# Performance work log

Measured on AMD Instinct MI355X. Metric: run time of the kernel, lower is better.

## Reference

```python
import jax, jax.numpy as jnp
import numpy as np

N_NODES = 50000


def gcn_conv(x, W, b, src, dst, n_nodes):
    # Linear transform first (PyG GCNConv): [N, out]
    h = x @ W
    # Add self-loops
    loop = jnp.arange(n_nodes, dtype=src.dtype)
    s = jnp.concatenate([src, loop])
    d = jnp.concatenate([dst, loop])
    # Symmetric normalization: deg counted at destination with unit weights
    deg = jax.ops.segment_sum(jnp.ones_like(d, dtype=h.dtype), d, num_segments=n_nodes)
    dinv = jnp.where(deg > 0, jax.lax.rsqrt(deg), 0.0)
    norm = dinv[s] * dinv[d]  # [E+N]
    # Gather source features, scale, scatter-add to destinations
    msgs = h[s] * norm[:, None]
    out = jax.ops.segment_sum(msgs, d, num_segments=n_nodes)
    return out + b


def setup_inputs() -> dict:
    key = jax.random.key(0)
    k1, k2, k3, k4, k5 = jax.random.split(key, 5)
    in_c, out_c = 512, 128
    x = jax.random.normal(k1, (N_NODES, in_c), dtype=jnp.float32)
    edge_index = jax.random.randint(k2, (2, 800000), 0, N_NODES, dtype=jnp.int64)
    glorot = 1.0 / np.sqrt(in_c)
    W_mu = jax.random.uniform(k3, (in_c, out_c), jnp.float32, -glorot, glorot)
    W_logstd = jax.random.uniform(k4, (in_c, out_c), jnp.float32, -glorot, glorot)
    b_mu = jnp.zeros((out_c,), jnp.float32)
    b_logstd = jnp.zeros((out_c,), jnp.float32)
    return {"x": x, "edge_index": edge_index, "W_mu": W_mu, "b_mu": b_mu,
            "W_logstd": W_logstd, "b_logstd": b_logstd}


def reference(x, edge_index, W_mu, b_mu, W_logstd, b_logstd):
    src, dst = edge_index[0], edge_index[1]
    mu = gcn_conv(x, W_mu, b_mu, src, dst, N_NODES)
    logstd = gcn_conv(x, W_logstd, b_logstd, src, dst, N_NODES)
    return mu, logstd
```

## Files before the change

### kernel.cpp

```cpp
#include <hip/hip_runtime.h>

#define NN 50000
#define NE 800000
#define KC 512
#define OC 256
#define NB_SCAN 196

typedef float f32x4 __attribute__((ext_vector_type(4)));
typedef short bf16x8 __attribute__((ext_vector_type(8)));

__device__ __forceinline__ unsigned f2bf(float f) {
    union { float f; unsigned u; } v; v.f = f;
    return (v.u + 0x7FFFu + ((v.u >> 16) & 1u)) >> 16;
}
__device__ __forceinline__ float bf2f(unsigned short b) {
    union { unsigned u; float f; } v; v.u = ((unsigned)b) << 16;
    return v.f;
}

__global__ __launch_bounds__(256) void count_deg_kernel(const int* __restrict__ ei,
                                                        int* __restrict__ deg) {
    int e = blockIdx.x * 256 + threadIdx.x;
    if (e < NE) atomicAdd(&deg[ei[NE + e]], 1);
}

__global__ __launch_bounds__(256) void scan_part_kernel(const int* __restrict__ deg,
                                                        int* __restrict__ partial) {
    int tid = threadIdx.x;
    int i = blockIdx.x * 256 + tid;
    int v = (i < NN) ? deg[i] : 0;
#pragma unroll
    for (int off = 32; off > 0; off >>= 1) v += __shfl_down(v, off, 64);
    __shared__ int wsum[4];
    if ((tid & 63) == 0) wsum[tid >> 6] = v;
    __syncthreads();
    if (tid == 0) partial[blockIdx.x] = wsum[0] + wsum[1] + wsum[2] + wsum[3];
}

__global__ __launch_bounds__(256) void scan_block_kernel(const int* __restrict__ partial,
                                                         int* __restrict__ blockoff) {
    __shared__ int lds[256];
    int tid = threadIdx.x;
    int v = (tid < NB_SCAN) ? partial[tid] : 0;
    lds[tid] = v;
    __syncthreads();
    for (int off = 1; off < 256; off <<= 1) {
        int t = (tid >= off) ? lds[tid - off] : 0;
        __syncthreads();
        lds[tid] += t;
        __syncthreads();
    }
    if (tid < NB_SCAN) blockoff[tid] = lds[tid] - v;
}

__global__ __launch_bounds__(256) void scan_apply_kernel(const int* __restrict__ deg,
                                                         const int* __restrict__ blockoff,
                                                         int* __restrict__ row_start,
                                                         int* __restrict__ cursor,
                                                         float* __restrict__ dinv) {
    int tid = threadIdx.x;
    int lane = tid & 63;
    int w = tid >> 6;
    int i = blockIdx.x * 256 + tid;
    int d = (i < NN) ? deg[i] : 0;
    int v = d;
#pragma unroll
    for (int off = 1; off < 64; off <<= 1) {
        int t = __shfl_up(v, off, 64);
        if (lane >= off) v += t;
    }
    __shared__ int wsum[4];
    if (lane == 63) wsum[w] = v;
    __syncthreads();
    int wof = 0;
    for (int k = 0; k < w; ++k) wof += wsum[k];
    int excl = blockoff[blockIdx.x] + wof + v - d;
    if (i < NN) {
        row_start[i] = excl;
        cursor[i] = excl;
        dinv[i] = rsqrtf((float)(d + 1));
    }
    if (i == NN - 1) row_start[NN] = excl + d;
}

__global__ __launch_bounds__(256) void scatter_kernel(const int* __restrict__ ei,
                                                      int* __restrict__ cursor,
                                                      int* __restrict__ csr_src) {
    int e = blockIdx.x * 256 + threadIdx.x;
    if (e < NE) {
        int d = ei[NE + e];
        int pos = atomicAdd(&cursor[d], 1);
        csr_src[pos] = ei[e];
    }
}

__global__ __launch_bounds__(256) void convw_kernel(const float* __restrict__ Wmu,
                                                    const float* __restrict__ Wls,
                                                    uint4* __restrict__ Wc) {
    int idx = blockIdx.x * 256 + threadIdx.x;
    int kb = idx >> 10;
    int rem = idx & 1023;
    int wf = rem >> 6;
    int lane = rem & 63;
    int g4 = lane >> 4;
    int i16 = lane & 15;
    int col = (wf >> 2) * 64 + (wf & 3) * 16 + i16;
    int k0 = kb * 32 + g4 * 8;
    const float* Wsrc = (col < 128) ? (Wmu + col) : (Wls + (col - 128));
    unsigned o[4];
#pragma unroll
    for (int p = 0; p < 4; ++p) {
        float lo = Wsrc[(size_t)(k0 + 2 * p) * 128];
        float hi = Wsrc[(size_t)(k0 + 2 * p + 1) * 128];
        o[p] = f2bf(lo) | (f2bf(hi) << 16);
    }
    uint4 v;
    v.x = o[0]; v.y = o[1]; v.z = o[2]; v.w = o[3];
    Wc[idx] = v;
}

__global__ __launch_bounds__(256, 8) void gemm_kernel(const float* __restrict__ x,
                                                      const uint4* __restrict__ Wc,
                                                      const float* __restrict__ dinv,
                                                      unsigned short* __restrict__ hs) {
    __shared__ __align__(16) float Af[2][32 * 64];

    int tid = threadIdx.x;
    int lane = tid & 63;
    int w = tid >> 6;
    int r0 = blockIdx.x * 32;
    int i16 = lane & 15;
    int g4 = lane >> 4;

    const float* srcp[2];
#pragma unroll
    for (int j = 0; j < 2; ++j) {
        int r = (w * 2 + j) * 4 + (lane >> 4);
        int gr = r0 + r;
        if (gr > NN - 1) gr = NN - 1;
        int cp = (lane & 15) >> 1;
        int mp = (lane & 1) * 4;
        int c = cp ^ (r & 7);
        int m = mp ^ (((r >> 3) & 1) * 4);
        srcp[j] = x + (size_t)gr * KC + c * 8 + m;
    }
    auto dmaA = [&](int buf, int S) {
#pragma unroll
        for (int j = 0; j < 2; ++j) {
            __builtin_amdgcn_global_load_lds(
                (const __attribute__((address_space(1))) void*)(srcp[j] + S * 64),
                (__attribute__((address_space(3))) void*)&Af[buf][(w * 2 + j) * 256], 16, 0, 0);
        }
    };

    auto readA = [&](int buf, int ks, int fr) -> bf16x8 {
        int r = fr * 16 + i16;
        int c = ks * 4 + g4;
        int cc = c ^ (r & 7);
        int mo = ((r >> 3) & 1) * 4;
        const float* p = &Af[buf][r * 64 + cc * 8];
        f32x4 lo = *(const f32x4*)(p + mo);
        f32x4 hi = *(const f32x4*)(p + (mo ^ 4));
        unsigned o0, o1, o2, o3;
        asm("v_cvt_pk_bf16_f32 %0, %1, %2" : "=v"(o0) : "v"(lo.x), "v"(lo.y));
        asm("v_cvt_pk_bf16_f32 %0, %1, %2" : "=v"(o1) : "v"(lo.z), "v"(lo.w));
        asm("v_cvt_pk_bf16_f32 %0, %1, %2" : "=v"(o2) : "v"(hi.x), "v"(hi.y));
        asm("v_cvt_pk_bf16_f32 %0, %1, %2" : "=v"(o3) : "v"(hi.z), "v"(hi.w));
        union { unsigned u[4]; bf16x8 v; } res;
        res.u[0] = o0; res.u[1] = o1; res.u[2] = o2; res.u[3] = o3;
        return res.v;
    };

    const uint4* wbase = Wc + (size_t)(w * 4) * 64 + lane;
    uint4 bb[2][4];
    auto loadB = [&](int dbuf, int kb) {
#pragma unroll
        for (int fc = 0; fc < 4; ++fc) bb[dbuf][fc] = wbase[kb * 1024 + fc * 64];
    };

    f32x4 acc[2][4];
    f32x4 zz = {0.f, 0.f, 0.f, 0.f};
#pragma unroll
    for (int a = 0; a < 2; ++a)
#pragma unroll
        for (int b = 0; b < 4; ++b) acc[a][b] = zz;

    dmaA(0, 0);
    loadB(0, 0);
    __syncthreads();

#pragma unroll
    for (int S = 0; S < 8; ++S) {
        if (S < 7) dmaA((S + 1) & 1, S + 1);
#pragma unroll
        for (int ks = 0; ks < 2; ++ks) {
            const int kb = S * 2 + ks;
            const int cur = kb & 1;
            if (kb < 15) loadB(cur ^ 1, kb + 1);
            bf16x8 af0 = readA(S & 1, ks, 0);
            bf16x8 af1 = readA(S & 1, ks, 1);
#pragma unroll
            for (int fc = 0; fc < 4; ++fc) {
                bf16x8 bfrag = *(const bf16x8*)&bb[cur][fc];
                acc[0][fc] = __builtin_amdgcn_mfma_f32_16x16x32_bf16(af0, bfrag, acc[0][fc], 0, 0, 0);
                acc[1][fc] = __builtin_amdgcn_mfma_f32_16x16x32_bf16(af1, bfrag, acc[1][fc], 0, 0, 0);
            }
        }
        if (S < 7) __syncthreads();
    }

#pragma unroll
    for (int fr = 0; fr < 2; ++fr) {
#pragma unroll
        for (int r = 0; r < 4; ++r) {
            int gr = r0 + fr * 16 + g4 * 4 + r;
            if (gr < NN) {
                float dv = dinv[gr];
#pragma unroll
                for (int fc = 0; fc < 4; ++fc) {
                    int col = w * 64 + fc * 16 + i16;
                    hs[(size_t)gr * OC + col] = (unsigned short)f2bf(acc[fr][fc][r] * dv);
                }
            }
        }
    }
}

__global__ __launch_bounds__(256) void aggregate_kernel(const unsigned short* __restrict__ hs,
                                                        const int* __restrict__ row_start,
                                                        const int* __restrict__ csr_src,
                                                        const float* __restrict__ dinv,
                                                        const float* __restrict__ bmu,
                                                        const float* __restrict__ bls,
                                                        float* __restrict__ out) {
    int tid = threadIdx.x;
    int lane = tid & 63;
    int node = blockIdx.x * 4 + (tid >> 6);

    const unsigned short* hrow = hs + lane * 4;
    float acc0, acc1, acc2, acc3;
    {
        ushort4 v = *(const ushort4*)&hrow[(size_t)node * OC];
        acc0 = bf2f(v.x);
        acc1 = bf2f(v.y);
        acc2 = bf2f(v.z);
        acc3 = bf2f(v.w);
    }
    int rs = row_start[node], re = row_start[node + 1];
    int e = rs;
    for (; e + 8 <= re; e += 8) {
        int s[8];
#pragma unroll
        for (int q = 0; q < 8; ++q) s[q] = csr_src[e + q];
        ushort4 v[8];
#pragma unroll
        for (int q = 0; q < 8; ++q) v[q] = *(const ushort4*)&hrow[(size_t)s[q] * OC];
#pragma unroll
        for (int q = 0; q < 8; ++q) {
            acc0 += bf2f(v[q].x);
            acc1 += bf2f(v[q].y);
            acc2 += bf2f(v[q].z);
            acc3 += bf2f(v[q].w);
        }
    }
    if (e + 4 <= re) {
        int s[4];
#pragma unroll
        for (int q = 0; q < 4; ++q) s[q] = csr_src[e + q];
        ushort4 v[4];
#pragma unroll
        for (int q = 0; q < 4; ++q) v[q] = *(const ushort4*)&hrow[(size_t)s[q] * OC];
#pragma unroll
        for (int q = 0; q < 4; ++q) {
            acc0 += bf2f(v[q].x);
            acc1 += bf2f(v[q].y);
            acc2 += bf2f(v[q].z);
            acc3 += bf2f(v[q].w);
        }
        e += 4;
    }
    for (; e < re; ++e) {
        int s0 = csr_src[e];
        ushort4 v0 = *(const ushort4*)&hrow[(size_t)s0 * OC];
        acc0 += bf2f(v0.x);
        acc1 += bf2f(v0.y);
        acc2 += bf2f(v0.z);
        acc3 += bf2f(v0.w);
    }
    float dn = dinv[node];
    if (lane < 32) {
        f32x4 b = *(const f32x4*)&bmu[lane * 4];
        f32x4 r;
        r.x = acc0 * dn + b.x;
        r.y = acc1 * dn + b.y;
        r.z = acc2 * dn + b.z;
        r.w = acc3 * dn + b.w;
        __builtin_nontemporal_store(r, (f32x4*)(out + (size_t)node * 128 + lane * 4));
    } else {
        f32x4 b = *(const f32x4*)&bls[(lane - 32) * 4];
        f32x4 r;
        r.x = acc0 * dn + b.x;
        r.y = acc1 * dn + b.y;
        r.z = acc2 * dn + b.z;
        r.w = acc3 * dn + b.w;
        __builtin_nontemporal_store(
            r, (f32x4*)(out + (size_t)NN * 128 + (size_t)node * 128 + (lane - 32) * 4));
    }
}

extern "C" void kernel_launch(void* const* d_in, const int* in_sizes, int n_in,
                              void* d_out, int out_size, void* d_ws, size_t ws_size,
                              hipStream_t stream) {
    const float* x = (const float*)d_in[0];
    const int* ei = (const int*)d_in[1];
    const float* Wmu = (const float*)d_in[2];
    const float* bmu = (const float*)d_in[3];
    const float* Wls = (const float*)d_in[4];
    const float* bls = (const float*)d_in[5];
    float* out = (float*)d_out;

    char* ws = (char*)d_ws;
    size_t off = 0;
    auto alloc = [&](size_t bytes) {
        void* p = ws + off;
        off += (bytes + 255) & ~(size_t)255;
        return p;
    };
    unsigned short* hs = (unsigned short*)alloc((size_t)NN * OC * sizeof(unsigned short));
    uint4* Wc = (uint4*)alloc((size_t)16384 * 16);
    int* deg = (int*)alloc((size_t)NN * sizeof(int));
    int* row_start = (int*)alloc((size_t)(NN + 1) * sizeof(int));
    int* cursor = (int*)alloc((size_t)NN * sizeof(int));
    int* csr_src = (int*)alloc((size_t)NE * sizeof(int));
    float* dinv = (float*)alloc((size_t)NN * sizeof(float));
    int* partial = (int*)alloc((size_t)NB_SCAN * sizeof(int));
    int* blockoff = (int*)alloc((size_t)NB_SCAN * sizeof(int));

    hipMemsetAsync(deg, 0, (size_t)NN * sizeof(int), stream);

    count_deg_kernel<<<(NE + 255) / 256, 256, 0, stream>>>(ei, deg);
    scan_part_kernel<<<NB_SCAN, 256, 0, stream>>>(deg, partial);
    scan_block_kernel<<<1, 256, 0, stream>>>(partial, blockoff);
    scan_apply_kernel<<<NB_SCAN, 256, 0, stream>>>(deg, blockoff, row_start, cursor, dinv);
    scatter_kernel<<<(NE + 255) / 256, 256, 0, stream>>>(ei, cursor, csr_src);
    convw_kernel<<<64, 256, 0, stream>>>(Wmu, Wls, Wc);
    gemm_kernel<<<(NN + 31) / 32, 256, 0, stream>>>(x, Wc, dinv, hs);
    aggregate_kernel<<<NN / 4, 256, 0, stream>>>(hs, row_start, csr_src, dinv, bmu, bls, out);
}
```

Baseline: 204.0 us.

## Load GEMM A fragments directly from global into registers, dropping LDS staging

The GEMM kernel no longer stages x tiles through shared memory with global_load_lds and barriers. Each wave now loads its own A fragments straight from global memory into registers, double-buffered across k-steps alongside the B fragments, and converts them to bf16 before the MFMA. This removes the LDS traffic and the block-wide syncs, but all four waves now load the same A rows redundantly, so more global/L2 traffic. Register pressure also rises, and launch bounds are relaxed from 8 to 4 waves-per-EU to accommodate it.

```diff
diff --git a/kernel.cpp b/kernel.cpp
--- a/kernel.cpp
+++ b/kernel.cpp
@@ -119,12 +119,10 @@
     Wc[idx] = v;
 }
 
-__global__ __launch_bounds__(256, 8) void gemm_kernel(const float* __restrict__ x,
+__global__ __launch_bounds__(256, 4) void gemm_kernel(const float* __restrict__ x,
                                                       const uint4* __restrict__ Wc,
                                                       const float* __restrict__ dinv,
                                                       unsigned short* __restrict__ hs) {
-    __shared__ __align__(16) float Af[2][32 * 64];
-
     int tid = threadIdx.x;
     int lane = tid & 63;
     int w = tid >> 6;
@@ -132,35 +130,28 @@
     int i16 = lane & 15;
     int g4 = lane >> 4;
 
-    const float* srcp[2];
-#pragma unroll
-    for (int j = 0; j < 2; ++j) {
-        int r = (w * 2 + j) * 4 + (lane >> 4);
-        int gr = r0 + r;
-        if (gr > NN - 1) gr = NN - 1;
-        int cp = (lane & 15) >> 1;
-        int mp = (lane & 1) * 4;
-        int c = cp ^ (r & 7);
-        int m = mp ^ (((r >> 3) & 1) * 4);
-        srcp[j] = x + (size_t)gr * KC + c * 8 + m;
-    }
-    auto dmaA = [&](int buf, int S) {
-#pragma unroll
-        for (int j = 0; j < 2; ++j) {
-            __builtin_amdgcn_global_load_lds(
-                (const __attribute__((address_space(1))) void*)(srcp[j] + S * 64),
-                (__attribute__((address_space(3))) void*)&Af[buf][(w * 2 + j) * 256], 16, 0, 0);
-        }
+    int gr0 = r0 + i16;
+    if (gr0 > NN - 1) gr0 = NN - 1;
+    int gr1 = r0 + 16 + i16;
+    if (gr1 > NN - 1) gr1 = NN - 1;
+    const float* xg0 = x + (size_t)gr0 * KC + g4 * 8;
+    const float* xg1 = x + (size_t)gr1 * KC + g4 * 8;
+    const uint4* wbase = Wc + (size_t)(w * 4) * 64 + lane;
+
+    f32x4 a0l[2], a0h[2], a1l[2], a1h[2];
+    uint4 bb[2][4];
+
+    auto loadA = [&](int buf, int kb) {
+        a0l[buf] = *(const f32x4*)(xg0 + kb * 32);
+        a0h[buf] = *(const f32x4*)(xg0 + kb * 32 + 4);
+        a1l[buf] = *(const f32x4*)(xg1 + kb * 32);
+        a1h[buf] = *(const f32x4*)(xg1 + kb * 32 + 4);
     };
-
-    auto readA = [&](int buf, int ks, int fr) -> bf16x8 {
-        int r = fr * 16 + i16;
-        int c = ks * 4 + g4;
-        int cc = c ^ (r & 7);
-        int mo = ((r >> 3) & 1) * 4;
-        const float* p = &Af[buf][r * 64 + cc * 8];
-        f32x4 lo = *(const f32x4*)(p + mo);
-        f32x4 hi = *(const f32x4*)(p + (mo ^ 4));
+    auto loadB = [&](int buf, int kb) {
+#pragma unroll
+        for (int fc = 0; fc < 4; ++fc) bb[buf][fc] = wbase[kb * 1024 + fc * 64];
+    };
+    auto cvtA = [&](f32x4 lo, f32x4 hi) -> bf16x8 {
         unsigned o0, o1, o2, o3;
         asm("v_cvt_pk_bf16_f32 %0, %1, %2" : "=v"(o0) : "v"(lo.x), "v"(lo.y));
         asm("v_cvt_pk_bf16_f32 %0, %1, %2" : "=v"(o1) : "v"(lo.z), "v"(lo.w));
@@ -171,13 +162,6 @@
         return res.v;
     };
 
-    const uint4* wbase = Wc + (size_t)(w * 4) * 64 + lane;
-    uint4 bb[2][4];
-    auto loadB = [&](int dbuf, int kb) {
-#pragma unroll
-        for (int fc = 0; fc < 4; ++fc) bb[dbuf][fc] = wbase[kb * 1024 + fc * 64];
-    };
-
     f32x4 acc[2][4];
     f32x4 zz = {0.f, 0.f, 0.f, 0.f};
 #pragma unroll
@@ -185,28 +169,29 @@
 #pragma unroll
         for (int b = 0; b < 4; ++b) acc[a][b] = zz;
 
-    dmaA(0, 0);
+    loadA(0, 0);
     loadB(0, 0);
-    __syncthreads();
-
-#pragma unroll
-    for (int S = 0; S < 8; ++S) {
-        if (S < 7) dmaA((S + 1) & 1, S + 1);
-#pragma unroll
-        for (int ks = 0; ks < 2; ++ks) {
-            const int kb = S * 2 + ks;
-            const int cur = kb & 1;
-            if (kb < 15) loadB(cur ^ 1, kb + 1);
-            bf16x8 af0 = readA(S & 1, ks, 0);
-            bf16x8 af1 = readA(S & 1, ks, 1);
-#pragma unroll
-            for (int fc = 0; fc < 4; ++fc) {
-                bf16x8 bfrag = *(const bf16x8*)&bb[cur][fc];
-                acc[0][fc] = __builtin_amdgcn_mfma_f32_16x16x32_bf16(af0, bfrag, acc[0][fc], 0, 0, 0);
-                acc[1][fc] = __builtin_amdgcn_mfma_f32_16x16x32_bf16(af1, bfrag, acc[1][fc], 0, 0, 0);
+
+#pragma unroll
+    for (int kb = 0; kb < 16; ++kb) {
+        const int cur = kb & 1;
+        if (kb < 15) {
+            loadA(cur ^ 1, kb + 1);
+            loadB(cur ^ 1, kb + 1);
+        }
+        bf16x8 af0 = cvtA(a0l[cur], a0h[cur]);
+        bf16x8 af1 = cvtA(a1l[cur], a1h[cur]);
+#pragma unroll
+        for (int fc = 0; fc < 4; ++fc) {
+            bf16x8 bfrag;
+            {
+                union { uint4 u; bf16x8 v; } cvt;
+                cvt.u = bb[cur][fc];
+                bfrag = cvt.v;
             }
-        }
-        if (S < 7) __syncthreads();
+            acc[0][fc] = __builtin_amdgcn_mfma_f32_16x16x32_bf16(af0, bfrag, acc[0][fc], 0, 0, 0);
+            acc[1][fc] = __builtin_amdgcn_mfma_f32_16x16x32_bf16(af1, bfrag, acc[1][fc], 0, 0, 0);
+        }
     }
 
 #pragma unroll
```

Result: slower. 229.0 us (+12.2%).
